# Kernel tuning notes

Hardware: AMD Instinct MI355X
Metric: run time of the kernel (lower is better)

The kernel has to match this reference:

```python
import jax, jax.numpy as jnp
import numpy as np

B, T, CIN, HID, OUT, H, W = 8, 8, 128, 64, 64, 32, 32


def _conv(x, w, b):
    # x: [B, C, H, W], w: [O, C, kh, kw] -> SAME-padded conv, stride 1
    y = jax.lax.conv_general_dilated(x, w, (1, 1), "SAME",
                                     dimension_numbers=("NCHW", "OIHW", "NCHW"))
    return y + b[None, :, None, None]


def _layer_dir(xs, w_ih, w_hh, b_ih, b_hh, reverse):
    # xs: [T, B, C, H, W]; one direction of a ConvLSTM layer; returns hs [T, B, HID, H, W]
    b, hh_, ww_ = xs.shape[1], xs.shape[3], xs.shape[4]
    h0 = jnp.zeros((b, HID, hh_, ww_), xs.dtype)

    def step(carry, x):
        h, c = carry
        gates = _conv(x, w_ih, b_ih) + _conv(h, w_hh, b_hh)  # [B, 4*HID, H, W]
        i, f, g, o = jnp.split(gates, 4, axis=1)
        c = jax.nn.sigmoid(f) * c + jax.nn.sigmoid(i) * jnp.tanh(g)
        h = jax.nn.sigmoid(o) * jnp.tanh(c)
        return (h, c), h

    _, hs = jax.lax.scan(step, (h0, h0), xs, reverse=reverse)
    return hs


def _forward(features, w_ih0f, w_hh0f, b_ih0f, b_hh0f,
             w_ih0r, w_hh0r, b_ih0r, b_hh0r,
             w_ih1f, w_hh1f, b_ih1f, b_hh1f,
             w_ih1r, w_hh1r, b_ih1r, b_hh1r,
             w_out, b_out):
    xs = jnp.transpose(features, (1, 0, 2, 3, 4))  # [T, B, C, H, W]
    # layer 0, both directions (scan reverse=True aligns outputs to original time order)
    hf = _layer_dir(xs, w_ih0f, w_hh0f, b_ih0f, b_hh0f, False)
    hr = _layer_dir(xs, w_ih0r, w_hh0r, b_ih0r, b_hh0r, True)
    xs1 = jnp.concatenate([hf, hr], axis=2)  # [T, B, 2*HID, H, W] (dropout is identity at eval)
    # layer 1
    hf1 = _layer_dir(xs1, w_ih1f, w_hh1f, b_ih1f, b_hh1f, False)
    hr1 = _layer_dir(xs1, w_ih1r, w_hh1r, b_ih1r, b_hh1r, True)
    last = jnp.concatenate([hf1[-1], hr1[-1]], axis=1)  # output[:, -1] -> [B, 2*HID, H, W]
    return jax.nn.relu(_conv(last, w_out, b_out))


def setup_inputs() -> dict:
    key = jax.random.key(0)
    ks = jax.random.split(key, 24)
    G = 4 * HID
    p = lambda k, s: jax.random.normal(k, s, jnp.float32) * 0.05
    d = {"features": jax.random.normal(ks[0], (B, T, CIN, H, W), jnp.float32)}
    i = 1
    for l, cin in ((0, CIN), (1, 2 * HID)):
        for dr in ("f", "r"):
            d[f"w_ih{l}{dr}"] = p(ks[i], (G, cin, 3, 3)); i += 1
            d[f"w_hh{l}{dr}"] = p(ks[i], (G, HID, 3, 3)); i += 1
            d[f"b_ih{l}{dr}"] = p(ks[i], (G,)); i += 1
            d[f"b_hh{l}{dr}"] = p(ks[i], (G,)); i += 1
    d["w_out"] = p(ks[i], (OUT, 2 * HID, 1, 1)); i += 1
    d["b_out"] = p(ks[i], (OUT,))
    return d


def reference(features, w_ih0f, w_hh0f, b_ih0f, b_hh0f,
              w_ih0r, w_hh0r, b_ih0r, b_hh0r,
              w_ih1f, w_hh1f, b_ih1f, b_hh1f,
              w_ih1r, w_hh1r, b_ih1r, b_hh1r,
              w_out, b_out):
    return _forward(features, w_ih0f, w_hh0f, b_ih0f, b_hh0f,
                    w_ih0r, w_hh0r, b_ih0r, b_hh0r,
                    w_ih1f, w_hh1f, b_ih1f, b_hh1f,
                    w_ih1r, w_hh1r, b_ih1r, b_hh1r,
                    w_out, b_out)
```

## Files before the change

### kernel.cpp

```cpp
#include <hip/hip_runtime.h>
#include <math.h>
#include <stdint.h>


typedef __attribute__((ext_vector_type(8))) short short8;
typedef __attribute__((ext_vector_type(4))) float float4v;

namespace {
constexpr int IMG = 34 * 34 * 64;
constexpr size_t SLOTI = 16ull * IMG;
constexpr int ROWB = 34 * 128;
constexpr int PADB = 8192;
}
template <int N> struct IC { static constexpr int v = N; };

__device__ __forceinline__ uint16_t bf16_rne(float x) {
  uint32_t u = __builtin_bit_cast(uint32_t, x);
  return (uint16_t)((u + 0x7FFFu + ((u >> 16) & 1u)) >> 16);
}
__device__ __forceinline__ float bf16_to_f(uint16_t h) {
  uint32_t u = ((uint32_t)h) << 16;
  return __builtin_bit_cast(float, u);
}

__device__ __forceinline__ void gl_lds16(const void* g, void* l) {
  __builtin_amdgcn_global_load_lds(
      (const __attribute__((address_space(1))) void*)g,
      (__attribute__((address_space(3))) void*)l, 16, 0, 0);
}

__global__ void pack_features(const float* __restrict__ f, uint16_t* __restrict__ out) {
  const size_t i = (size_t)blockIdx.x * 256 + threadIdx.x;
  const int blk_s = (int)(i & 7);
  size_t pp = i >> 3;
  const int px = (int)(pp % 34); pp /= 34;
  const int yy = (int)(pp % 34); pp /= 34;
  const int cg = (int)(pp & 3);
  const int bt = (int)(pp >> 2);
  const int b = bt & 7, t = bt >> 3;
  const int blk = blk_s ^ (px & 7);
  const int pl = blk >> 2, kg = blk & 3;
  short8 sv;
  if (px == 0 || px == 33 || yy == 0 || yy == 33) {
    #pragma unroll
    for (int j = 0; j < 8; ++j) sv[j] = 0;
  } else {
    const int x = px - 1, y = yy - 1;
    #pragma unroll
    for (int j = 0; j < 8; ++j) {
      const int ch = cg * 32 + kg * 8 + j;
      const float fv = f[(((size_t)b * 8 + t) * 128 + ch) * 1024 + y * 32 + x];
      const uint16_t hi = bf16_rne(fv);
      sv[j] = (short)(pl ? bf16_rne(fv - bf16_to_f(hi)) : hi);
    }
  }
  *(short8*)(out + i * 8) = sv;
}

struct WPackArgs {
  const float* wih[4]; const float* whh[4];
  const float* bih[4]; const float* bhh[4];
  uint32_t* wp; float* bp;
};
__global__ void pack_weights(WPackArgs A) {
  const int combo = blockIdx.y;
  const int idx = blockIdx.x * 256 + threadIdx.x;
  const int q = idx & 4095;
  const int rest = idx >> 12;
  const int nt = rest & 1;
  const int ct = rest >> 1;
  const int tap = ct % 9, cg = ct / 9;
  const int w2 = q & 3;
  const int b8s = (q >> 2) & 7;
  const int hcp = (q >> 5) & 15;
  const int g = (q >> 9) & 3;
  const int pl = (q >> 11) & 1;
  const int b8 = b8s ^ (hcp & 7);
  const int kg = b8 & 3;
  const int hcl = hcp * 2 + (b8 >> 2);
  const int n = g * 64 + nt * 32 + hcl;
  const float* wih = A.wih[combo];
  const float* whh = A.whh[combo];
  uint32_t out = 0;
  #pragma unroll
  for (int e = 0; e < 2; ++e) {
    const int ch = cg * 32 + kg * 8 + w2 * 2 + e;
    const float wv = (ch < 128) ? wih[((size_t)n * 128 + ch) * 9 + tap]
                                : whh[((size_t)n * 64 + (ch - 128)) * 9 + tap];
    const uint16_t hi = bf16_rne(wv);
    const uint16_t v = pl ? bf16_rne(wv - bf16_to_f(hi)) : hi;
    out |= ((uint32_t)v) << (16 * e);
  }
  A.wp[(size_t)combo * 442368 + idx] = out;
  if (idx < 256) A.bp[combo * 256 + idx] = A.bih[combo][idx] + A.bhh[combo][idx];
}

struct StepArgs {
  const uint16_t* in0; const uint16_t* in1; const uint16_t* in2;
  int nc0, nc1, nc2;
  const uint32_t* W;
  const float* bias;
  float* cbuf;
  uint16_t* himg;
  float* hf32;
};

__global__ __launch_bounds__(512, 2) void conv_lstm_step(StepArgs A0, StepArgs A1) {
  extern __shared__ char smem[];
  char* Asm_ = smem;
  char* Wsm_ = smem + 65536;

  const StepArgs a = (blockIdx.z == 0) ? A0 : A1;
  const int bx = blockIdx.x;
  const int nt = bx & 1;
  const int band = (bx >> 1) & 7;
  const int b = bx >> 4;
  const int y0 = band * 4;
  const int tid = threadIdx.x;
  const int lane = tid & 63;
  const int w = tid >> 6;
  const int m15 = lane & 15;
  const int kg = lane >> 4;
  const int r = w & 3;
  const int hcg = w >> 2;

  int offA[2][3][2];
  #pragma unroll
  for (int xh = 0; xh < 2; ++xh)
    #pragma unroll
    for (int kx = 0; kx < 3; ++kx)
      #pragma unroll
      for (int pl = 0; pl < 2; ++pl) {
        const int px = xh * 16 + kx + m15;
        const int sw = (pl * 4 + kg) ^ (px & 7);
        offA[xh][kx][pl] = r * ROWB + px * 128 + sw * 16;
      }
  int offW[2][4];
  {
    const int hcp = hcg * 8 + (m15 >> 1);
    const int b8 = kg + 4 * (m15 & 1);
    #pragma unroll
    for (int pl = 0; pl < 2; ++pl)
      #pragma unroll
      for (int g = 0; g < 4; ++g)
        offW[pl][g] = (((pl * 4 + g) * 16 + hcp) * 8 + (b8 ^ (hcp & 7))) * 16;
  }

  const int ncg = a.nc0 + a.nc1 + a.nc2;
  auto abase = [&](int cg) -> const char* {
    const uint16_t* t;
    if (cg < a.nc0) t = a.in0 + ((size_t)b * a.nc0 + cg) * IMG;
    else if (cg < a.nc0 + a.nc1) t = a.in1 + ((size_t)b * a.nc1 + (cg - a.nc0)) * IMG;
    else t = a.in2 + ((size_t)b * a.nc2 + (cg - a.nc0 - a.nc1)) * IMG;
    return (const char*)t + (size_t)y0 * ROWB;
  };
  auto stageA = [&](int cgi, int par) {
    const char* g = abase(cgi);
    char* d = Asm_ + par * 32768;
    #pragma unroll
    for (int j = 0; j < 4; ++j)
      gl_lds16(g + (size_t)(4 * w + j) * 1024 + lane * 16, d + (4 * w + j) * 1024);
  };
  auto stageW = [&](int cgs, int taps, int slot) {
    const char* g = (const char*)a.W + ((size_t)((cgs * 9 + taps) * 2 + nt) << 14);
    char* d = Wsm_ + slot * 16384;
    #pragma unroll
    for (int j = 0; j < 2; ++j)
      gl_lds16(g + (size_t)(2 * w + j) * 1024 + lane * 16, d + (2 * w + j) * 1024);
  };

  float4v acc[2][4];
  #pragma unroll
  for (int xh = 0; xh < 2; ++xh)
    #pragma unroll
    for (int g = 0; g < 4; ++g) acc[xh][g] = (float4v){0.f, 0.f, 0.f, 0.f};

  stageA(0, 0);
  stageW(0, 0, 0);
  stageW(0, 1, 1);

  for (int cg = 0; cg < ncg; ++cg) {
    auto tap_body = [&](auto tapc) {
      constexpr int TAP = decltype(tapc)::v;
      constexpr int CNT = (TAP == 1 || TAP == 2) ? 6 : 2;
      asm volatile("s_waitcnt vmcnt(%0)\n\ts_barrier" :: "n"(CNT) : "memory");
      const int lin = cg * 9 + TAP;
      {
        const int l2 = lin + 2;
        int cgs = l2 / 9;
        const int taps = l2 % 9;
        if (cgs >= ncg) cgs = 0;
        stageW(cgs, taps, l2 % 3);
      }
      if (TAP == 0) {
        const int nx = (cg + 1 < ncg) ? cg + 1 : 0;
        stageA(nx, (cg + 1) & 1);
      }
      constexpr int ky = TAP / 3, kx = TAP % 3;
      const char* Ab = Asm_ + (cg & 1) * 32768 + ky * ROWB;
      const char* Wb = Wsm_ + (lin % 3) * 16384;
      short8 af[2][2];
      #pragma unroll
      for (int xh = 0; xh < 2; ++xh)
        #pragma unroll
        for (int pl = 0; pl < 2; ++pl)
          af[xh][pl] = *(const short8*)(Ab + offA[xh][kx][pl]);
      short8 wfr[2][4];
      #pragma unroll
      for (int pl = 0; pl < 2; ++pl)
        #pragma unroll
        for (int g = 0; g < 4; ++g)
          wfr[pl][g] = *(const short8*)(Wb + offW[pl][g]);
      #pragma unroll
      for (int xh = 0; xh < 2; ++xh)
        #pragma unroll
        for (int g = 0; g < 4; ++g) {
          acc[xh][g] = __builtin_amdgcn_mfma_f32_16x16x32_bf16(af[xh][0], wfr[0][g], acc[xh][g], 0, 0, 0);
          acc[xh][g] = __builtin_amdgcn_mfma_f32_16x16x32_bf16(af[xh][0], wfr[1][g], acc[xh][g], 0, 0, 0);
          acc[xh][g] = __builtin_amdgcn_mfma_f32_16x16x32_bf16(af[xh][1], wfr[0][g], acc[xh][g], 0, 0, 0);
        }
    };
    tap_body(IC<0>{}); tap_body(IC<1>{}); tap_body(IC<2>{});
    tap_body(IC<3>{}); tap_body(IC<4>{}); tap_body(IC<5>{});
    tap_body(IC<6>{}); tap_body(IC<7>{}); tap_body(IC<8>{});
  }
  asm volatile("s_waitcnt vmcnt(0)" ::: "memory");

  const int hcl = hcg * 16 + m15;
  const int hc = nt * 32 + hcl;
  const int y = y0 + r;
  float bi[4];
  #pragma unroll
  for (int g = 0; g < 4; ++g) bi[g] = a.bias[g * 64 + hc];
  float* crow = a.cbuf + ((size_t)(b * 64 + hc)) * 1024 + y * 32;
  float* hrow = a.hf32 ? a.hf32 + ((size_t)(b * 64 + hc)) * 1024 + y * 32 : nullptr;
  uint16_t* hb = a.himg ? a.himg + ((size_t)(b * 2 + nt)) * IMG : nullptr;
  const int kgb = hcl >> 3, jj = hcl & 7;
  #pragma unroll
  for (int xh = 0; xh < 2; ++xh) {
    const int x0 = xh * 16 + kg * 4;
    float4v cv = *(float4v*)(crow + x0);
    float4v cn, hn;
    #pragma unroll
    for (int q = 0; q < 4; ++q) {
      const float ig = 1.f / (1.f + expf(-(acc[xh][0][q] + bi[0])));
      const float fg = 1.f / (1.f + expf(-(acc[xh][1][q] + bi[1])));
      const float gg = tanhf(acc[xh][2][q] + bi[2]);
      const float og = 1.f / (1.f + expf(-(acc[xh][3][q] + bi[3])));
      const float c2 = fg * cv[q] + ig * gg;
      cn[q] = c2;
      hn[q] = og * tanhf(c2);
    }
    *(float4v*)(crow + x0) = cn;
    if (hrow) *(float4v*)(hrow + x0) = hn;
    if (hb) {
      #pragma unroll
      for (int q = 0; q < 4; ++q) {
        const int px = x0 + q + 1;
        const int sw = px & 7;
        const uint16_t hi = bf16_rne(hn[q]);
        const uint16_t lo = bf16_rne(hn[q] - bf16_to_f(hi));
        const size_t p16 = ((size_t)(y + 1) * 34 + px) * 64;
        hb[p16 + (size_t)(kgb ^ sw) * 8 + jj] = hi;
        hb[p16 + (size_t)((4 + kgb) ^ sw) * 8 + jj] = lo;
      }
    }
  }
  if (hb) {
    {
      const int rr = tid >> 7;
      const int hlf = (tid >> 6) & 1;
      const int jx = tid & 63;
      hb[((size_t)(y0 + 1 + rr) * 34 + hlf * 33) * 64 + jx] = 0;
    }
    if (band == 0) for (int i = tid; i < 2176; i += 512) hb[i] = 0;
    if (band == 7) for (int i = tid; i < 2176; i += 512) hb[(size_t)33 * 2176 + i] = 0;
  }
}

__global__ void final_conv(const float* __restrict__ h1f_last, const float* __restrict__ h1r_last,
                           const float* __restrict__ wout, const float* __restrict__ bout,
                           float* __restrict__ out) {
  __shared__ float Ws[16 * 128];
  const int oq = blockIdx.y;
  for (int i = threadIdx.x; i < 16 * 128; i += 256) Ws[i] = wout[oq * 16 * 128 + i];
  __syncthreads();
  const int gp = blockIdx.x * 256 + threadIdx.x;
  const int b = gp >> 10, p = gp & 1023;
  float acc[16];
  #pragma unroll
  for (int o = 0; o < 16; ++o) acc[o] = bout[oq * 16 + o];
  for (int c = 0; c < 128; ++c) {
    const float xv = (c < 64) ? h1f_last[((size_t)b * 64 + c) * 1024 + p]
                              : h1r_last[((size_t)b * 64 + (c - 64)) * 1024 + p];
    #pragma unroll
    for (int o = 0; o < 16; ++o) acc[o] = fmaf(xv, Ws[o * 128 + c], acc[o]);
  }
  #pragma unroll
  for (int o = 0; o < 16; ++o) {
    const float v = acc[o];
    out[((size_t)b * 64 + oq * 16 + o) * 1024 + p] = v > 0.f ? v : 0.f;
  }
}

extern "C" void kernel_launch(void* const* d_in, const int* in_sizes, int n_in,
                              void* d_out, int out_size, void* d_ws, size_t ws_size,
                              hipStream_t stream) {
  char* p = (char*)d_ws;
  uint16_t* featImg = (uint16_t*)p; p += (size_t)8 * 8 * 4 * IMG * 2 + PADB;
  uint32_t* WP = (uint32_t*)p;      p += (size_t)4 * 442368 * 4;
  float* bp = (float*)p;            p += 4096;
  uint16_t* hf0i = (uint16_t*)p;    p += (size_t)9 * SLOTI * 2 + PADB;
  uint16_t* hr0i = (uint16_t*)p;    p += (size_t)9 * SLOTI * 2 + PADB;
  uint16_t* h1fi = (uint16_t*)p;    p += (size_t)2 * SLOTI * 2 + PADB;
  float* c0f = (float*)p;           p += (size_t)4 * 2097152;
  float* c0r = c0f + 524288;
  float* c1f = c0r + 524288;
  float* c1r = c1f + 524288;
  float* h1f8 = (float*)p;          p += 2097152;
  float* h1r8 = (float*)p;          p += 2097152;

  hipMemsetAsync(c0f, 0, (size_t)4 * 2097152, stream);
  hipMemsetAsync(hf0i, 0, (size_t)SLOTI * 2, stream);
  hipMemsetAsync(hr0i + (size_t)8 * SLOTI, 0, (size_t)SLOTI * 2, stream);
  hipMemsetAsync(h1fi, 0, (size_t)SLOTI * 2, stream);

  pack_features<<<dim3(9248), 256, 0, stream>>>((const float*)d_in[0], featImg);

  WPackArgs wa;
  for (int combo = 0; combo < 4; ++combo) {
    const int base = 1 + combo * 4;
    wa.wih[combo] = (const float*)d_in[base];
    wa.whh[combo] = (const float*)d_in[base + 1];
    wa.bih[combo] = (const float*)d_in[base + 2];
    wa.bhh[combo] = (const float*)d_in[base + 3];
  }
  wa.wp = WP; wa.bp = bp;
  pack_weights<<<dim3(1728, 4), 256, 0, stream>>>(wa);

  constexpr int DYN_LDS = 114688;
  (void)hipFuncSetAttribute((const void*)conv_lstm_step,
                            hipFuncAttributeMaxDynamicSharedMemorySize, DYN_LDS);

  auto mk = [&](const uint16_t* i0, int n0, const uint16_t* i1, int n1,
                const uint16_t* i2, int n2, int combo, float* cb,
                uint16_t* himg, float* hf32) {
    StepArgs s;
    s.in0 = i0; s.in1 = i1; s.in2 = i2;
    s.nc0 = n0; s.nc1 = n1; s.nc2 = n2;
    s.W = WP + (size_t)combo * 442368; s.bias = bp + combo * 256;
    s.cbuf = cb; s.himg = himg; s.hf32 = hf32;
    return s;
  };

  for (int k = 0; k < 8; ++k) {
    const int tr = 7 - k;
    StepArgs f = mk(featImg + (size_t)k * 8 * 4 * IMG, 4,
                    hf0i + (size_t)k * SLOTI, 2, nullptr, 0,
                    0, c0f, hf0i + (size_t)(k + 1) * SLOTI, nullptr);
    StepArgs r = mk(featImg + (size_t)tr * 8 * 4 * IMG, 4,
                    hr0i + (size_t)(tr + 1) * SLOTI, 2, nullptr, 0,
                    1, c0r, hr0i + (size_t)tr * SLOTI, nullptr);
    conv_lstm_step<<<dim3(128, 1, 2), 512, DYN_LDS, stream>>>(f, r);
  }

  for (int t = 0; t < 8; ++t) {
    uint16_t* himg = (t < 7) ? h1fi + (size_t)((t + 1) & 1) * SLOTI : nullptr;
    float* hf32 = (t == 7) ? h1f8 : nullptr;
    StepArgs s = mk(hf0i + (size_t)(t + 1) * SLOTI, 2, hr0i + (size_t)t * SLOTI, 2,
                    h1fi + (size_t)(t & 1) * SLOTI, 2, 2, c1f, himg, hf32);
    if (t == 0) {
      StepArgs rv = mk(hf0i + (size_t)8 * SLOTI, 2, hr0i + (size_t)7 * SLOTI, 2,
                       nullptr, 0, 3, c1r, nullptr, h1r8);
      conv_lstm_step<<<dim3(128, 1, 2), 512, DYN_LDS, stream>>>(s, rv);
    } else {
      conv_lstm_step<<<dim3(128, 1, 1), 512, DYN_LDS, stream>>>(s, s);
    }
  }

  final_conv<<<dim3(32, 4), 256, 0, stream>>>(
      h1f8, h1r8, (const float*)d_in[17], (const float*)d_in[18], (float*)d_out);
}
```

Before: 776.1 us.

## Stage weights per kernel row with double buffering to cut barriers

```diff
diff --git a/kernel.cpp b/kernel.cpp
--- a/kernel.cpp
+++ b/kernel.cpp
@@ -161,12 +161,16 @@
     for (int j = 0; j < 4; ++j)
       gl_lds16(g + (size_t)(4 * w + j) * 1024 + lane * 16, d + (4 * w + j) * 1024);
   };
-  auto stageW = [&](int cgs, int taps, int slot) {
-    const char* g = (const char*)a.W + ((size_t)((cgs * 9 + taps) * 2 + nt) << 14);
-    char* d = Wsm_ + slot * 16384;
-    #pragma unroll
-    for (int j = 0; j < 2; ++j)
-      gl_lds16(g + (size_t)(2 * w + j) * 1024 + lane * 16, d + (2 * w + j) * 1024);
+  auto stageWrow = [&](int cgs, int jr, int buf) {
+    char* dbase = Wsm_ + buf * 49152;
+    #pragma unroll
+    for (int t3 = 0; t3 < 3; ++t3) {
+      const char* g = (const char*)a.W + ((size_t)((cgs * 9 + jr * 3 + t3) * 2 + nt) << 14);
+      char* d = dbase + t3 * 16384;
+      #pragma unroll
+      for (int jj = 0; jj < 2; ++jj)
+        gl_lds16(g + (size_t)(2 * w + jj) * 1024 + lane * 16, d + (2 * w + jj) * 1024);
+    }
   };
 
   float4v acc[2][4];
@@ -176,53 +180,51 @@
     for (int g = 0; g < 4; ++g) acc[xh][g] = (float4v){0.f, 0.f, 0.f, 0.f};
 
   stageA(0, 0);
-  stageW(0, 0, 0);
-  stageW(0, 1, 1);
+  stageWrow(0, 0, 0);
 
   for (int cg = 0; cg < ncg; ++cg) {
-    auto tap_body = [&](auto tapc) {
-      constexpr int TAP = decltype(tapc)::v;
-      constexpr int CNT = (TAP == 1 || TAP == 2) ? 6 : 2;
+    auto row_body = [&](auto jc) {
+      constexpr int J = decltype(jc)::v;
+      constexpr int CNT = (J == 1) ? 4 : 0;
       asm volatile("s_waitcnt vmcnt(%0)\n\ts_barrier" :: "n"(CNT) : "memory");
-      const int lin = cg * 9 + TAP;
+      const int i = cg * 3 + J;
       {
-        const int l2 = lin + 2;
-        int cgs = l2 / 9;
-        const int taps = l2 % 9;
-        if (cgs >= ncg) cgs = 0;
-        stageW(cgs, taps, l2 % 3);
-      }
-      if (TAP == 0) {
+        int cgs = cg + (J == 2 ? 1 : 0);
+        int jn = (J == 2) ? 0 : J + 1;
+        if (cgs >= ncg) { cgs = 0; jn = 0; }
+        stageWrow(cgs, jn, (i + 1) & 1);
+      }
+      if (J == 0) {
         const int nx = (cg + 1 < ncg) ? cg + 1 : 0;
         stageA(nx, (cg + 1) & 1);
       }
-      constexpr int ky = TAP / 3, kx = TAP % 3;
-      const char* Ab = Asm_ + (cg & 1) * 32768 + ky * ROWB;
-      const char* Wb = Wsm_ + (lin % 3) * 16384;
-      short8 af[2][2];
-      #pragma unroll
-      for (int xh = 0; xh < 2; ++xh)
+      const char* Ab = Asm_ + (cg & 1) * 32768 + J * ROWB;
+      const char* Wb = Wsm_ + (i & 1) * 49152;
+      #pragma unroll
+      for (int kx = 0; kx < 3; ++kx) {
+        short8 af[2][2];
+        #pragma unroll
+        for (int xh = 0; xh < 2; ++xh)
+          #pragma unroll
+          for (int pl = 0; pl < 2; ++pl)
+            af[xh][pl] = *(const short8*)(Ab + offA[xh][kx][pl]);
+        short8 wfr[2][4];
         #pragma unroll
         for (int pl = 0; pl < 2; ++pl)
-          af[xh][pl] = *(const short8*)(Ab + offA[xh][kx][pl]);
-      short8 wfr[2][4];
-      #pragma unroll
-      for (int pl = 0; pl < 2; ++pl)
+          #pragma unroll
+          for (int g = 0; g < 4; ++g)
+            wfr[pl][g] = *(const short8*)(Wb + kx * 16384 + offW[pl][g]);
         #pragma unroll
-        for (int g = 0; g < 4; ++g)
-          wfr[pl][g] = *(const short8*)(Wb + offW[pl][g]);
-      #pragma unroll
-      for (int xh = 0; xh < 2; ++xh)
-        #pragma unroll
-        for (int g = 0; g < 4; ++g) {
-          acc[xh][g] = __builtin_amdgcn_mfma_f32_16x16x32_bf16(af[xh][0], wfr[0][g], acc[xh][g], 0, 0, 0);
-          acc[xh][g] = __builtin_amdgcn_mfma_f32_16x16x32_bf16(af[xh][0], wfr[1][g], acc[xh][g], 0, 0, 0);
-          acc[xh][g] = __builtin_amdgcn_mfma_f32_16x16x32_bf16(af[xh][1], wfr[0][g], acc[xh][g], 0, 0, 0);
-        }
+        for (int xh = 0; xh < 2; ++xh)
+          #pragma unroll
+          for (int g = 0; g < 4; ++g) {
+            acc[xh][g] = __builtin_amdgcn_mfma_f32_16x16x32_bf16(af[xh][0], wfr[0][g], acc[xh][g], 0, 0, 0);
+            acc[xh][g] = __builtin_amdgcn_mfma_f32_16x16x32_bf16(af[xh][0], wfr[1][g], acc[xh][g], 0, 0, 0);
+            acc[xh][g] = __builtin_amdgcn_mfma_f32_16x16x32_bf16(af[xh][1], wfr[0][g], acc[xh][g], 0, 0, 0);
+          }
+      }
     };
-    tap_body(IC<0>{}); tap_body(IC<1>{}); tap_body(IC<2>{});
-    tap_body(IC<3>{}); tap_body(IC<4>{}); tap_body(IC<5>{});
-    tap_body(IC<6>{}); tap_body(IC<7>{}); tap_body(IC<8>{});
+    row_body(IC<0>{}); row_body(IC<1>{}); row_body(IC<2>{});
   }
   asm volatile("s_waitcnt vmcnt(0)" ::: "memory");
 
@@ -338,7 +340,7 @@
   wa.wp = WP; wa.bp = bp;
   pack_weights<<<dim3(1728, 4), 256, 0, stream>>>(wa);
 
-  constexpr int DYN_LDS = 114688;
+  constexpr int DYN_LDS = 163840;
   (void)hipFuncSetAttribute((const void*)conv_lstm_step,
                             hipFuncAttributeMaxDynamicSharedMemorySize, DYN_LDS);
 
```

Measured after the change: 762.2 us. About the same (-1.8%).

## Software-pipeline LDS fragment reads with MFMA and deepen weight ring buffer

Applied to the files above, without the earlier changes.

```diff
diff --git a/kernel.cpp b/kernel.cpp
--- a/kernel.cpp
+++ b/kernel.cpp
@@ -161,70 +161,94 @@
     for (int j = 0; j < 4; ++j)
       gl_lds16(g + (size_t)(4 * w + j) * 1024 + lane * 16, d + (4 * w + j) * 1024);
   };
-  auto stageW = [&](int cgs, int taps, int slot) {
-    const char* g = (const char*)a.W + ((size_t)((cgs * 9 + taps) * 2 + nt) << 14);
+  const char* const wbeg = (const char*)a.W + (size_t)nt * 16384;
+  const char* const wend = (const char*)a.W + (size_t)ncg * 9 * 32768;
+  const char* wsrc = wbeg;
+  auto stageW = [&](int slot) {
     char* d = Wsm_ + slot * 16384;
     #pragma unroll
     for (int j = 0; j < 2; ++j)
-      gl_lds16(g + (size_t)(2 * w + j) * 1024 + lane * 16, d + (2 * w + j) * 1024);
-  };
-
+      gl_lds16(wsrc + (size_t)(2 * w + j) * 1024 + lane * 16, d + (2 * w + j) * 1024);
+    wsrc += 32768;
+    if (wsrc >= wend) wsrc = wbeg;
+  };
+
+  short8 af[2][2][2];
+  short8 wf[2][2][4];
   float4v acc[2][4];
   #pragma unroll
   for (int xh = 0; xh < 2; ++xh)
     #pragma unroll
     for (int g = 0; g < 4; ++g) acc[xh][g] = (float4v){0.f, 0.f, 0.f, 0.f};
 
+  auto issue_reads = [&](auto sc, auto tc, const char* Apar, const char* Wb) {
+    constexpr int S = decltype(sc)::v;
+    constexpr int TAP = decltype(tc)::v;
+    constexpr int ky = TAP / 3, kx = TAP % 3;
+    const char* Ab = Apar + ky * ROWB;
+    #pragma unroll
+    for (int xh = 0; xh < 2; ++xh)
+      #pragma unroll
+      for (int pl = 0; pl < 2; ++pl)
+        af[S][xh][pl] = *(const short8*)(Ab + offA[xh][kx][pl]);
+    #pragma unroll
+    for (int pl = 0; pl < 2; ++pl)
+      #pragma unroll
+      for (int g = 0; g < 4; ++g)
+        wf[S][pl][g] = *(const short8*)(Wb + offW[pl][g]);
+  };
+  auto run_mfma = [&](auto sc) {
+    constexpr int S = decltype(sc)::v;
+    #pragma unroll
+    for (int xh = 0; xh < 2; ++xh)
+      #pragma unroll
+      for (int g = 0; g < 4; ++g) {
+        acc[xh][g] = __builtin_amdgcn_mfma_f32_16x16x32_bf16(af[S][xh][0], wf[S][0][g], acc[xh][g], 0, 0, 0);
+        acc[xh][g] = __builtin_amdgcn_mfma_f32_16x16x32_bf16(af[S][xh][0], wf[S][1][g], acc[xh][g], 0, 0, 0);
+        acc[xh][g] = __builtin_amdgcn_mfma_f32_16x16x32_bf16(af[S][xh][1], wf[S][0][g], acc[xh][g], 0, 0, 0);
+      }
+  };
+
   stageA(0, 0);
-  stageW(0, 0, 0);
-  stageW(0, 1, 1);
-
-  for (int cg = 0; cg < ncg; ++cg) {
-    auto tap_body = [&](auto tapc) {
-      constexpr int TAP = decltype(tapc)::v;
+  stageW(0); stageW(1); stageW(2);
+  asm volatile("s_waitcnt vmcnt(4)" ::: "memory");
+  __builtin_amdgcn_s_barrier();
+  issue_reads(IC<0>{}, IC<0>{}, Asm_, Wsm_);
+
+  auto pair = [&](auto pbc, int cgbase) {
+    constexpr int PB = decltype(pbc)::v;
+    auto body = [&](auto tc2) {
+      constexpr int t = decltype(tc2)::v;
+      constexpr int TAP = t % 9;
       constexpr int CNT = (TAP == 1 || TAP == 2) ? 6 : 2;
-      asm volatile("s_waitcnt vmcnt(%0)\n\ts_barrier" :: "n"(CNT) : "memory");
-      const int lin = cg * 9 + TAP;
-      {
-        const int l2 = lin + 2;
-        int cgs = l2 / 9;
-        const int taps = l2 % 9;
-        if (cgs >= ncg) cgs = 0;
-        stageW(cgs, taps, l2 % 3);
-      }
+      constexpr int S = t & 1;
+      asm volatile("s_waitcnt vmcnt(%0)" :: "n"(CNT) : "memory");
+      __builtin_amdgcn_s_barrier();
+      stageW((2 * PB + t + 3) & 3);
       if (TAP == 0) {
+        const int cg = cgbase + t / 9;
         const int nx = (cg + 1 < ncg) ? cg + 1 : 0;
         stageA(nx, (cg + 1) & 1);
       }
-      constexpr int ky = TAP / 3, kx = TAP % 3;
-      const char* Ab = Asm_ + (cg & 1) * 32768 + ky * ROWB;
-      const char* Wb = Wsm_ + (lin % 3) * 16384;
-      short8 af[2][2];
-      #pragma unroll
-      for (int xh = 0; xh < 2; ++xh)
-        #pragma unroll
-        for (int pl = 0; pl < 2; ++pl)
-          af[xh][pl] = *(const short8*)(Ab + offA[xh][kx][pl]);
-      short8 wfr[2][4];
-      #pragma unroll
-      for (int pl = 0; pl < 2; ++pl)
-        #pragma unroll
-        for (int g = 0; g < 4; ++g)
-          wfr[pl][g] = *(const short8*)(Wb + offW[pl][g]);
-      #pragma unroll
-      for (int xh = 0; xh < 2; ++xh)
-        #pragma unroll
-        for (int g = 0; g < 4; ++g) {
-          acc[xh][g] = __builtin_amdgcn_mfma_f32_16x16x32_bf16(af[xh][0], wfr[0][g], acc[xh][g], 0, 0, 0);
-          acc[xh][g] = __builtin_amdgcn_mfma_f32_16x16x32_bf16(af[xh][0], wfr[1][g], acc[xh][g], 0, 0, 0);
-          acc[xh][g] = __builtin_amdgcn_mfma_f32_16x16x32_bf16(af[xh][1], wfr[0][g], acc[xh][g], 0, 0, 0);
-        }
+      issue_reads(IC<S ^ 1>{}, IC<(t + 1) % 9>{},
+                  Asm_ + (((t + 1) / 9) & 1) * 32768,
+                  Wsm_ + ((2 * PB + t + 1) & 3) * 16384);
+      asm volatile("s_waitcnt lgkmcnt(12)" ::: "memory");
+      __builtin_amdgcn_sched_barrier(0);
+      __builtin_amdgcn_s_setprio(1);
+      run_mfma(IC<S>{});
+      __builtin_amdgcn_s_setprio(0);
     };
-    tap_body(IC<0>{}); tap_body(IC<1>{}); tap_body(IC<2>{});
-    tap_body(IC<3>{}); tap_body(IC<4>{}); tap_body(IC<5>{});
-    tap_body(IC<6>{}); tap_body(IC<7>{}); tap_body(IC<8>{});
-  }
-  asm volatile("s_waitcnt vmcnt(0)" ::: "memory");
+    body(IC<0>{});  body(IC<1>{});  body(IC<2>{});  body(IC<3>{});  body(IC<4>{});
+    body(IC<5>{});  body(IC<6>{});  body(IC<7>{});  body(IC<8>{});  body(IC<9>{});
+    body(IC<10>{}); body(IC<11>{}); body(IC<12>{}); body(IC<13>{}); body(IC<14>{});
+    body(IC<15>{}); body(IC<16>{}); body(IC<17>{});
+  };
+  pair(IC<0>{}, 0);
+  pair(IC<1>{}, 2);
+  if (ncg == 6) pair(IC<0>{}, 4);
+
+  asm volatile("s_waitcnt vmcnt(0) lgkmcnt(0)" ::: "memory");
 
   const int hcl = hcg * 16 + m15;
   const int hc = nt * 32 + hcl;
@@ -338,7 +362,7 @@
   wa.wp = WP; wa.bp = bp;
   pack_weights<<<dim3(1728, 4), 256, 0, stream>>>(wa);
 
-  constexpr int DYN_LDS = 114688;
+  constexpr int DYN_LDS = 131072;
   (void)hipFuncSetAttribute((const void*)conv_lstm_step,
                             hipFuncAttributeMaxDynamicSharedMemorySize, DYN_LDS);
 
```

Result: slower. 792.7 us (+2.1%).
